# Kernel optimization log

Hardware: AMD Instinct MI355X
Metric: run time of the kernel (lower is better)

## Reference

```python
import jax, jax.numpy as jnp
import numpy as np

H, W = 512, 1024
R = 5                      # circle_radius
K = 2 * R + 1              # circle_k_size = 11
NMS_K = 7                  # nms_kernel_size
TOP_K = 200

# static circle geometry (matches registered buffers)
_ky, _kx = np.mgrid[0:K, 0:K]
OFF_X = (_kx + 1 - (K + 1) // 2).astype(np.float32)  # circle_coords[0]
OFF_Y = (_ky + 1 - (K + 1) // 2).astype(np.float32)  # circle_coords[1]
_circle_dists = np.sqrt(OFF_X ** 2 + OFF_Y ** 2)
CIRCLE_MASK = (_circle_dists <= R).astype(np.float32)
N_CIRCLE = float(CIRCLE_MASK.sum())
CENTER_THRESH = float((_circle_dists * CIRCLE_MASK).sum() / N_CIRCLE + 0.5)


def setup_inputs() -> dict:
    key = jax.random.key(0)
    k1, k2 = jax.random.split(key)
    fg_pred = jax.random.uniform(k1, (1, 1, H, W), dtype=jnp.float32)
    center_regressions = jax.random.normal(k2, (1, 2, H, W), dtype=jnp.float32)
    return {"fg_pred": fg_pred, "center_regressions": center_regressions}


def _vote_map(center_regressions):
    """Circular-mask Hough voting error + 1, shape (B, H, W)."""
    B = center_regressions.shape[0]
    pad = K // 2
    rp = jnp.pad(center_regressions, ((0, 0), (0, 0), (pad, pad), (pad, pad)))
    err = jnp.zeros((B, H, W), jnp.float32)
    # loop over fixed 11x11 kernel taps (only the ~81 inside the circle)
    for iy in range(K):
        for ix in range(K):
            if CIRCLE_MASK[iy, ix] == 0.0:
                continue
            rx = rp[:, 0, iy:iy + H, ix:ix + W]
            ry = rp[:, 1, iy:iy + H, ix:ix + W]
            err = err + jnp.sqrt((OFF_X[iy, ix] - rx) ** 2 + (OFF_Y[iy, ix] - ry) ** 2)
    return err / N_CIRCLE + 1.0


def reference(fg_pred, center_regressions):
    B = fg_pred.shape[0]
    xs_grid = jnp.arange(1, W + 1, dtype=jnp.float32)[None, :]
    ys_grid = jnp.arange(1, H + 1, dtype=jnp.float32)[:, None]
    pred_x = xs_grid - center_regressions[:, 0]  # (B, H, W)
    pred_y = ys_grid - center_regressions[:, 1]
    things = fg_pred[:, 0] >= 0.5                # (B, H, W)

    vote = _vote_map(center_regressions)
    # NMS: -maxpool(-x) == minpool, torch pads with -inf for maxpool -> +inf here
    hp = NMS_K // 2
    pooled = jax.lax.reduce_window(vote, jnp.inf, jax.lax.min,
                                   (1, NMS_K, NMS_K), (1, 1, 1),
                                   [(0, 0), (hp, hp), (hp, hp)])
    vote = jnp.where(pooled == vote, vote, 0.0)
    vote = jnp.where(vote >= CENTER_THRESH, 0.0, vote)

    # get_centers: top_k smallest nonzero errors (padded with +inf / valid mask)
    flat = vote.reshape(B, H * W)
    cand = jnp.where(flat > 0.0, flat, jnp.inf)
    neg_err, idx = jax.lax.top_k(-cand, TOP_K)   # smallest errors, ascending
    cerr = -neg_err                              # (B, TOP_K)
    valid = jnp.isfinite(cerr)
    cy = (idx // W).astype(jnp.float32)          # 0-based rows (torch.nonzero)
    cx = (idx % W).astype(jnp.float32)

    # create_inst_maps: assign each pixel to nearest center (argmin over K centers)
    dist2 = (pred_x[..., None] - cx[:, None, None, :]) ** 2 + \
            (pred_y[..., None] - cy[:, None, None, :]) ** 2  # (B, H, W, TOP_K)
    dist2 = jnp.where(valid[:, None, None, :], dist2, jnp.inf)
    inst = jnp.argmin(dist2, axis=-1).astype(jnp.int32) + 1
    any_valid = valid.any(axis=1)
    inst = inst * things.astype(jnp.int32) * any_valid[:, None, None].astype(jnp.int32)

    coords = jnp.stack([cy, cx], axis=-1).astype(jnp.int32)  # (B, TOP_K, 2) as (y, x)
    cerr_out = jnp.where(valid, cerr, 0.0)
    return inst, coords, cerr_out
```

## Files before the change

kernel.cpp:

```cpp
#include <hip/hip_runtime.h>
#include <math.h>

#define HH 512
#define WW 1024
#define RR 5
#define KK 11
#define TOPK 200
#define MAXC 16384

#define BW 64
#define BH 16
#define TT 4
#define SROWS (BH + 10)
#define SCOLS (BW + 10)


__global__ __launch_bounds__(256) void vote_kernel(const float* __restrict__ cr,
                                                   float* __restrict__ vote,
                                                   int* __restrict__ meta) {
    __shared__ float2 s[SROWS][SCOLS + 2];
    const int tid = threadIdx.x;
    const int bx = blockIdx.x * BW, by = blockIdx.y * BH;

    if (bx == 0 && by == 0 && tid < 4) meta[tid] = 0;

    for (int l = tid; l < SROWS * SCOLS; l += 256) {
        int r = l / SCOLS, c = l % SCOLS;
        int gy = by - 5 + r, gx = bx - 5 + c;
        bool ok = (gy >= 0) && (gy < HH) && (gx >= 0) && (gx < WW);
        float vx = ok ? cr[gy * WW + gx] : 0.0f;
        float vy = ok ? cr[HH * WW + gy * WW + gx] : 0.0f;
        s[r][c] = make_float2(vx, vy);
    }
    __syncthreads();

    const int x = tid & 63;
    const int yt = tid >> 6;
    float a[TT] = {0.f, 0.f, 0.f, 0.f};
    float b[TT] = {0.f, 0.f, 0.f, 0.f};

    #pragma unroll
    for (int rr = 0; rr < TT + 10; ++rr) {
        #pragma unroll
        for (int ix = 0; ix < KK; ++ix) {
            const int ox = ix - 5;
            bool any = false;
            #pragma unroll
            for (int t = 0; t < TT; ++t) {
                const int oy = rr - 5 - t;
                if (oy >= -RR && oy <= RR && ox * ox + oy * oy <= RR * RR) any = true;
            }
            if (!any) continue;
            float2 v = s[yt * TT + rr][x + ix];
            #pragma unroll
            for (int t = 0; t < TT; ++t) {
                const int oy = rr - 5 - t;
                if (oy >= -RR && oy <= RR && ox * ox + oy * oy <= RR * RR) {
                    float dx = (float)ox - v.x;
                    float dy = (float)oy - v.y;
                    float sv = __builtin_amdgcn_sqrtf(fmaf(dy, dy, dx * dx));
                    if (ix & 1) b[t] += sv; else a[t] += sv;
                }
            }
        }
    }
    const int y0 = by + yt * TT;
    #pragma unroll
    for (int t = 0; t < TT; ++t)
        vote[(y0 + t) * WW + bx + x] = (a[t] + b[t]) / 81.0f + 1.0f;
}

__global__ __launch_bounds__(256) void nms_kernel(const float* __restrict__ vote,
                                                  float* __restrict__ cv, int* __restrict__ ci,
                                                  int* __restrict__ meta, float ct) {
    const int tid = threadIdx.x;
    const int x = blockIdx.x * 64 + (tid & 63);
    const int y0 = blockIdx.y * 16 + (tid >> 6) * 4;

    int xc[7];
    #pragma unroll
    for (int d = 0; d < 7; ++d) xc[d] = min(max(x + d - 3, 0), WW - 1);

    float r[10], c[4];
    #pragma unroll
    for (int j = 0; j < 10; ++j) {
        int yy = min(max(y0 + j - 3, 0), HH - 1);
        const float* row = vote + yy * WW;
        float m0 = fminf(row[xc[0]], row[xc[1]]);
        float m1 = fminf(row[xc[2]], row[xc[3]]);
        float m2 = fminf(row[xc[4]], row[xc[5]]);
        float m3 = row[xc[6]];
        if (j >= 3 && j < 7) c[j - 3] = row[xc[3]];
        r[j] = fminf(fminf(m0, m1), fminf(m2, m3));
    }
    float p[9], q4[7];
    #pragma unroll
    for (int j = 0; j < 9; ++j) p[j] = fminf(r[j], r[j + 1]);
    #pragma unroll
    for (int j = 0; j < 7; ++j) q4[j] = fminf(p[j], p[j + 2]);
    #pragma unroll
    for (int t = 0; t < 4; ++t) {
        float m = fminf(q4[t], q4[t + 3]);
        float v = c[t];
        if (v == m && v < ct) {
            int s = atomicAdd(&meta[0], 1);
            if (s < MAXC) { cv[s] = v; ci[s] = (y0 + t) * WW + x; }
        }
    }
}

__global__ __launch_bounds__(256) void inst_select_kernel(const float* __restrict__ fg,
                                                          const float* __restrict__ cr,
                                                          const float* __restrict__ cv,
                                                          const int* __restrict__ ci,
                                                          const int* __restrict__ meta,
                                                          float* __restrict__ out) {
    __shared__ float bv[256];
    __shared__ int bi[256];
    __shared__ int s_idx[TOPK];
    __shared__ float s_val[TOPK];
    __shared__ float s_selx[TOPK];
    __shared__ float s_sely[TOPK];
    const int tid = threadIdx.x;
    int M = meta[0];
    if (M > MAXC) M = MAXC;
    const int Mtop = (M < TOPK) ? M : TOPK;

    float lastv = -INFINITY;
    int lasti = -1;
    for (int k = 0; k < Mtop; ++k) {
        float bestv = INFINITY;
        int besti = 0x7fffffff;
        for (int j = tid; j < M; j += 256) {
            float cvj = cv[j];
            int cij = ci[j];
            if (cvj > lastv || (cvj == lastv && cij > lasti)) {
                if (cvj < bestv || (cvj == bestv && cij < besti)) { bestv = cvj; besti = cij; }
            }
        }
        bv[tid] = bestv; bi[tid] = besti;
        __syncthreads();
        for (int s = 128; s > 0; s >>= 1) {
            if (tid < s) {
                float ov = bv[tid + s]; int oi = bi[tid + s];
                if (ov < bv[tid] || (ov == bv[tid] && oi < bi[tid])) { bv[tid] = ov; bi[tid] = oi; }
            }
            __syncthreads();
        }
        lastv = bv[0]; lasti = bi[0];
        if (tid == 0) { s_val[k] = lastv; s_idx[k] = lasti; }
        __syncthreads();
    }

    for (int k = Mtop + tid; k < TOPK; k += 256) {
        int r = k - Mtop;
        int g = r, prev = -1;
        while (g != prev) {
            prev = g;
            int cnt = 0;
            for (int j = 0; j < M; ++j) cnt += (ci[j] <= g) ? 1 : 0;
            g = r + cnt;
        }
        s_idx[k] = g;
        s_val[k] = INFINITY;
    }
    __syncthreads();

    for (int k = tid; k < TOPK; k += 256) {
        int idx = s_idx[k];
        s_sely[k] = (float)(idx >> 10);
        s_selx[k] = (float)(idx & (WW - 1));
    }
    __syncthreads();

    if (blockIdx.x == 0) {
        for (int k = tid; k < TOPK; k += 256) {
            out[HH * WW + 2 * k]     = s_sely[k];
            out[HH * WW + 2 * k + 1] = s_selx[k];
            out[HH * WW + 2 * TOPK + k] = (k < Mtop) ? s_val[k] : 0.0f;
        }
    }

    int idx4 = blockIdx.x * 256 + tid;
    float4 o = make_float4(0.f, 0.f, 0.f, 0.f);
    if (M > 0) {
        int pix0 = idx4 * 4;
        int y = pix0 >> 10;
        float4 f = ((const float4*)fg)[idx4];
        float4 cx0 = ((const float4*)cr)[idx4];
        float4 cy0 = ((const float4*)(cr + HH * WW))[idx4];
        float fgv[4] = {f.x, f.y, f.z, f.w};
        float crx[4] = {cx0.x, cx0.y, cx0.z, cx0.w};
        float cry[4] = {cy0.x, cy0.y, cy0.z, cy0.w};
        float res[4];
        #pragma unroll
        for (int t = 0; t < 4; ++t) {
            res[t] = 0.f;
            if (fgv[t] >= 0.5f) {
                int x = (pix0 + t) & (WW - 1);
                float px = (float)(x + 1) - crx[t];
                float py = (float)(y + 1) - cry[t];
                float best = INFINITY;
                int bk = 0;
                for (int k = 0; k < Mtop; ++k) {
                    float ddx = px - s_selx[k];
                    float ddy = py - s_sely[k];
                    float d = ddx * ddx + ddy * ddy;
                    if (d < best) { best = d; bk = k; }
                }
                res[t] = (float)(bk + 1);
            }
        }
        o = make_float4(res[0], res[1], res[2], res[3]);
    }
    ((float4*)out)[idx4] = o;
}

extern "C" void kernel_launch(void* const* d_in, const int* in_sizes, int n_in,
                              void* d_out, int out_size, void* d_ws, size_t ws_size,
                              hipStream_t stream) {
    const float* fg = (const float*)d_in[0];
    const float* cr = (const float*)d_in[1];
    float* out = (float*)d_out;

    char* ws = (char*)d_ws;
    int* meta = (int*)ws;
    float* vote = (float*)(ws + 64);
    float* cv = (float*)(ws + 64 + 4 * HH * WW);
    int* ci = (int*)(ws + 64 + 4 * HH * WW + 4 * MAXC);

    double s = 0.0;
    int n = 0;
    for (int iy = 0; iy < KK; ++iy)
        for (int ix = 0; ix < KK; ++ix) {
            double dx = ix - RR, dy = iy - RR;
            double d = sqrt(dx * dx + dy * dy);
            if (d <= (double)RR) { s += d; n++; }
        }
    float ct = (float)(s / n + 0.5);

    dim3 vgrid(WW / BW, HH / BH);
    vote_kernel<<<vgrid, 256, 0, stream>>>(cr, vote, meta);
    dim3 ngrid(WW / 64, HH / 16);
    nms_kernel<<<ngrid, 256, 0, stream>>>(vote, cv, ci, meta, ct);
    inst_select_kernel<<<(HH * WW / 4) / 256, 256, 0, stream>>>(fg, cr, cv, ci, meta, out);
}
```

Before: 22.47 us.

## Fuse vote and NMS into one kernel with per-block candidate buckets

Merges the voting and 7x7 min-pool NMS kernels into one 512-thread kernel. It computes the vote map plus a 3-pixel halo in shared memory and runs NMS from LDS, so the full vote map never goes through global memory. Candidates go into per-block buckets through a shared atomic counter instead of a global one. The selection kernel prefix-sums the bucket counts and stages candidates in shared memory. The halo is recomputed per tile, and candidates are capped per block (160) and in total (1536), which could drop candidates compared with the old global cap.

```diff
diff --git a/kernel.cpp b/kernel.cpp
--- a/kernel.cpp
+++ b/kernel.cpp
@@ -6,27 +6,36 @@
 #define RR 5
 #define KK 11
 #define TOPK 200
-#define MAXC 16384
-
-#define BW 64
-#define BH 16
-#define TT 4
-#define SROWS (BH + 10)
-#define SCOLS (BW + 10)
-
-
-__global__ __launch_bounds__(256) void vote_kernel(const float* __restrict__ cr,
-                                                   float* __restrict__ vote,
-                                                   int* __restrict__ meta) {
-    __shared__ float2 s[SROWS][SCOLS + 2];
+
+#define TW 64
+#define TH 32
+#define SVH (TH + 6)
+#define SVW (TW + 6)
+#define CRH (TH + 16)
+#define CRW (TW + 16)
+#define CRHA 52
+#define MAXPB 160
+#define NBUCK 256
+#define CAP 1536
+
+
+__global__ __launch_bounds__(512) void vote_nms_kernel(const float* __restrict__ cr,
+                                                       float* __restrict__ gcv,
+                                                       int* __restrict__ gci,
+                                                       int* __restrict__ counts, float ct) {
+    __shared__ float2 s[CRHA][CRW + 2];
+    __shared__ float sv[SVH][SVW + 2];
+    __shared__ int lcnt;
+    __shared__ float lval[MAXPB];
+    __shared__ int lidx[MAXPB];
     const int tid = threadIdx.x;
-    const int bx = blockIdx.x * BW, by = blockIdx.y * BH;
-
-    if (bx == 0 && by == 0 && tid < 4) meta[tid] = 0;
-
-    for (int l = tid; l < SROWS * SCOLS; l += 256) {
-        int r = l / SCOLS, c = l % SCOLS;
-        int gy = by - 5 + r, gx = bx - 5 + c;
+    const int bx = blockIdx.x * TW, by = blockIdx.y * TH;
+    if (tid == 0) lcnt = 0;
+
+    for (int l = tid; l < CRHA * CRW; l += 512) {
+        int r = l / CRW, c = l % CRW;
+        int rs = min(r, CRH - 1);
+        int gy = by - 8 + rs, gx = bx - 8 + c;
         bool ok = (gy >= 0) && (gy < HH) && (gx >= 0) && (gx < WW);
         float vx = ok ? cr[gy * WW + gx] : 0.0f;
         float vy = ok ? cr[HH * WW + gy * WW + gx] : 0.0f;
@@ -34,87 +43,98 @@
     }
     __syncthreads();
 
-    const int x = tid & 63;
-    const int yt = tid >> 6;
-    float a[TT] = {0.f, 0.f, 0.f, 0.f};
-    float b[TT] = {0.f, 0.f, 0.f, 0.f};
-
-    #pragma unroll
-    for (int rr = 0; rr < TT + 10; ++rr) {
-        #pragma unroll
-        for (int ix = 0; ix < KK; ++ix) {
-            const int ox = ix - 5;
-            bool any = false;
+    const int col = tid % SVW;
+    const int grp = tid / SVW;
+    if (grp < 7) {
+        float a[6] = {0.f, 0.f, 0.f, 0.f, 0.f, 0.f};
+        float b[6] = {0.f, 0.f, 0.f, 0.f, 0.f, 0.f};
+        #pragma unroll
+        for (int rr = 0; rr < 16; ++rr) {
             #pragma unroll
-            for (int t = 0; t < TT; ++t) {
-                const int oy = rr - 5 - t;
-                if (oy >= -RR && oy <= RR && ox * ox + oy * oy <= RR * RR) any = true;
-            }
-            if (!any) continue;
-            float2 v = s[yt * TT + rr][x + ix];
-            #pragma unroll
-            for (int t = 0; t < TT; ++t) {
-                const int oy = rr - 5 - t;
-                if (oy >= -RR && oy <= RR && ox * ox + oy * oy <= RR * RR) {
-                    float dx = (float)ox - v.x;
-                    float dy = (float)oy - v.y;
-                    float sv = __builtin_amdgcn_sqrtf(fmaf(dy, dy, dx * dx));
-                    if (ix & 1) b[t] += sv; else a[t] += sv;
+            for (int ix = 0; ix < KK; ++ix) {
+                const int ox = ix - 5;
+                bool any = false;
+                #pragma unroll
+                for (int t = 0; t < 6; ++t) {
+                    const int oy = rr - 5 - t;
+                    if (oy >= -RR && oy <= RR && ox * ox + oy * oy <= RR * RR) any = true;
                 }
-            }
-        }
-    }
-    const int y0 = by + yt * TT;
-    #pragma unroll
-    for (int t = 0; t < TT; ++t)
-        vote[(y0 + t) * WW + bx + x] = (a[t] + b[t]) / 81.0f + 1.0f;
-}
-
-__global__ __launch_bounds__(256) void nms_kernel(const float* __restrict__ vote,
-                                                  float* __restrict__ cv, int* __restrict__ ci,
-                                                  int* __restrict__ meta, float ct) {
-    const int tid = threadIdx.x;
-    const int x = blockIdx.x * 64 + (tid & 63);
-    const int y0 = blockIdx.y * 16 + (tid >> 6) * 4;
-
-    int xc[7];
-    #pragma unroll
-    for (int d = 0; d < 7; ++d) xc[d] = min(max(x + d - 3, 0), WW - 1);
-
-    float r[10], c[4];
-    #pragma unroll
-    for (int j = 0; j < 10; ++j) {
-        int yy = min(max(y0 + j - 3, 0), HH - 1);
-        const float* row = vote + yy * WW;
-        float m0 = fminf(row[xc[0]], row[xc[1]]);
-        float m1 = fminf(row[xc[2]], row[xc[3]]);
-        float m2 = fminf(row[xc[4]], row[xc[5]]);
-        float m3 = row[xc[6]];
-        if (j >= 3 && j < 7) c[j - 3] = row[xc[3]];
-        r[j] = fminf(fminf(m0, m1), fminf(m2, m3));
-    }
-    float p[9], q4[7];
-    #pragma unroll
-    for (int j = 0; j < 9; ++j) p[j] = fminf(r[j], r[j + 1]);
-    #pragma unroll
-    for (int j = 0; j < 7; ++j) q4[j] = fminf(p[j], p[j + 2]);
-    #pragma unroll
-    for (int t = 0; t < 4; ++t) {
-        float m = fminf(q4[t], q4[t + 3]);
-        float v = c[t];
-        if (v == m && v < ct) {
-            int s = atomicAdd(&meta[0], 1);
-            if (s < MAXC) { cv[s] = v; ci[s] = (y0 + t) * WW + x; }
-        }
+                if (!any) continue;
+                float2 v = s[grp * 6 + rr][col + ix];
+                float dx = (float)ox - v.x;
+                float dx2 = dx * dx;
+                #pragma unroll
+                for (int t = 0; t < 6; ++t) {
+                    const int oy = rr - 5 - t;
+                    if (oy >= -RR && oy <= RR && ox * ox + oy * oy <= RR * RR) {
+                        float dy = (float)oy - v.y;
+                        float sq = __builtin_amdgcn_sqrtf(fmaf(dy, dy, dx2));
+                        if (ix & 1) b[t] += sq; else a[t] += sq;
+                    }
+                }
+            }
+        }
+        #pragma unroll
+        for (int t = 0; t < 6; ++t) {
+            int R = grp * 6 + t;
+            if (R < SVH) {
+                int gy = by - 3 + R, gx = bx - 3 + col;
+                bool in = (gy >= 0) && (gy < HH) && (gx >= 0) && (gx < WW);
+                sv[R][col] = in ? (a[t] + b[t]) / 81.0f + 1.0f : INFINITY;
+            }
+        }
+    }
+    __syncthreads();
+
+    {
+        const int x = tid & 63;
+        const int g = tid >> 6;
+        float r10[10], ctr[4];
+        #pragma unroll
+        for (int j = 0; j < 10; ++j) {
+            const float* row = &sv[g * 4 + j][x];
+            float m0 = fminf(row[0], row[1]);
+            float m1 = fminf(row[2], row[3]);
+            float m2 = fminf(row[4], row[5]);
+            float m3 = row[6];
+            if (j >= 3 && j < 7) ctr[j - 3] = row[3];
+            r10[j] = fminf(fminf(m0, m1), fminf(m2, m3));
+        }
+        float p[9], q[7];
+        #pragma unroll
+        for (int j = 0; j < 9; ++j) p[j] = fminf(r10[j], r10[j + 1]);
+        #pragma unroll
+        for (int j = 0; j < 7; ++j) q[j] = fminf(p[j], p[j + 2]);
+        #pragma unroll
+        for (int t = 0; t < 4; ++t) {
+            float m = fminf(q[t], q[t + 3]);
+            float v = ctr[t];
+            if (v == m && v < ct) {
+                int sp = atomicAdd(&lcnt, 1);
+                if (sp < MAXPB) { lval[sp] = v; lidx[sp] = (by + g * 4 + t) * WW + bx + x; }
+            }
+        }
+    }
+    __syncthreads();
+
+    int bkt = blockIdx.y * gridDim.x + blockIdx.x;
+    int cnt = min(lcnt, MAXPB);
+    if (tid == 0) counts[bkt] = cnt;
+    for (int i = tid; i < cnt; i += 512) {
+        gcv[bkt * MAXPB + i] = lval[i];
+        gci[bkt * MAXPB + i] = lidx[i];
     }
 }
 
 __global__ __launch_bounds__(256) void inst_select_kernel(const float* __restrict__ fg,
                                                           const float* __restrict__ cr,
-                                                          const float* __restrict__ cv,
-                                                          const int* __restrict__ ci,
-                                                          const int* __restrict__ meta,
+                                                          const float* __restrict__ gcv,
+                                                          const int* __restrict__ gci,
+                                                          const int* __restrict__ counts,
                                                           float* __restrict__ out) {
+    __shared__ int s_pre[NBUCK];
+    __shared__ float s_cv[CAP];
+    __shared__ int s_ci[CAP];
     __shared__ float bv[256];
     __shared__ int bi[256];
     __shared__ int s_idx[TOPK];
@@ -122,8 +142,26 @@
     __shared__ float s_selx[TOPK];
     __shared__ float s_sely[TOPK];
     const int tid = threadIdx.x;
-    int M = meta[0];
-    if (M > MAXC) M = MAXC;
+
+    int myc = counts[tid];
+    s_pre[tid] = myc;
+    __syncthreads();
+    #pragma unroll
+    for (int off = 1; off < NBUCK; off <<= 1) {
+        int add = (tid >= off) ? s_pre[tid - off] : 0;
+        __syncthreads();
+        s_pre[tid] += add;
+        __syncthreads();
+    }
+    int total = s_pre[NBUCK - 1];
+    int M = min(total, CAP);
+    int base = s_pre[tid] - myc;
+    for (int j = 0; j < myc; ++j) {
+        int p = base + j;
+        if (p < CAP) { s_cv[p] = gcv[tid * MAXPB + j]; s_ci[p] = gci[tid * MAXPB + j]; }
+    }
+    __syncthreads();
+
     const int Mtop = (M < TOPK) ? M : TOPK;
 
     float lastv = -INFINITY;
@@ -132,8 +170,8 @@
         float bestv = INFINITY;
         int besti = 0x7fffffff;
         for (int j = tid; j < M; j += 256) {
-            float cvj = cv[j];
-            int cij = ci[j];
+            float cvj = s_cv[j];
+            int cij = s_ci[j];
             if (cvj > lastv || (cvj == lastv && cij > lasti)) {
                 if (cvj < bestv || (cvj == bestv && cij < besti)) { bestv = cvj; besti = cij; }
             }
@@ -157,9 +195,9 @@
         int g = r, prev = -1;
         while (g != prev) {
             prev = g;
-            int cnt = 0;
-            for (int j = 0; j < M; ++j) cnt += (ci[j] <= g) ? 1 : 0;
-            g = r + cnt;
+            int cnt2 = 0;
+            for (int j = 0; j < M; ++j) cnt2 += (s_ci[j] <= g) ? 1 : 0;
+            g = r + cnt2;
         }
         s_idx[k] = g;
         s_val[k] = INFINITY;
@@ -224,10 +262,9 @@
     float* out = (float*)d_out;
 
     char* ws = (char*)d_ws;
-    int* meta = (int*)ws;
-    float* vote = (float*)(ws + 64);
-    float* cv = (float*)(ws + 64 + 4 * HH * WW);
-    int* ci = (int*)(ws + 64 + 4 * HH * WW + 4 * MAXC);
+    int* counts = (int*)ws;
+    float* gcv = (float*)(ws + 1024);
+    int* gci = (int*)(ws + 1024 + 4 * NBUCK * MAXPB);
 
     double s = 0.0;
     int n = 0;
@@ -239,9 +276,7 @@
         }
     float ct = (float)(s / n + 0.5);
 
-    dim3 vgrid(WW / BW, HH / BH);
-    vote_kernel<<<vgrid, 256, 0, stream>>>(cr, vote, meta);
-    dim3 ngrid(WW / 64, HH / 16);
-    nms_kernel<<<ngrid, 256, 0, stream>>>(vote, cv, ci, meta, ct);
-    inst_select_kernel<<<(HH * WW / 4) / 256, 256, 0, stream>>>(fg, cr, cv, ci, meta, out);
+    dim3 vgrid(WW / TW, HH / TH);
+    vote_nms_kernel<<<vgrid, 512, 0, stream>>>(cr, gcv, gci, counts, ct);
+    inst_select_kernel<<<(HH * WW / 4) / 256, 256, 0, stream>>>(fg, cr, gcv, gci, counts, out);
 }
```

Result: slower. 27.01 us (+20.2%).
